# Optimization experiments

Hardware: AMD Instinct MI355X
Metric: run time of the kernel (lower is better)

## Reference

```python
import jax, jax.numpy as jnp
from jax import lax
import numpy as np

B = 8192   # samples
L = 32     # predicted chars per sample (num_chars[i])
M = 32     # target labels per sample (num_labels[i])
C = 96     # character classes


def _edit_trace(pred, tgt):
    """Levenshtein DP + backtrace for one sample.
    pred: [L] int, tgt: [M] int.
    Returns (ti, tj, valid) of length L+M: 1-based (i,j) positions of the
    diagonal (match/substitute) moves on the optimal edit path, as emitted by
    distance_and_trace; valid masks non-diagonal / out-of-path steps."""
    Ls, Ms = pred.shape[0], tgt.shape[0]
    cost = (pred[:, None] != tgt[None, :]).astype(jnp.int32)  # [L,M]
    row0 = jnp.arange(Ms + 1, dtype=jnp.int32)

    def row_step(prev, crow):
        first = prev[0] + 1
        def col_step(left, z):
            up, diag, c = z
            v = jnp.minimum(jnp.minimum(up + 1, left + 1), diag + c)
            return v, v
        _, rest = lax.scan(col_step, first, (prev[1:], prev[:-1], crow))
        new = jnp.concatenate([first[None], rest])
        return new, new

    _, rows = lax.scan(row_step, row0, cost)
    D = jnp.concatenate([row0[None, :], rows], axis=0)  # [L+1, M+1]

    def bt_step(carry, _):
        i, j = carry
        c = cost[jnp.maximum(i - 1, 0), jnp.maximum(j - 1, 0)]
        dij = D[i, j]
        diag = (i > 0) & (j > 0) & (D[i - 1, j - 1] + c == dij)
        up = (~diag) & (i > 0) & (D[i - 1, j] + 1 == dij)
        left = (~diag) & (~up) & (j > 0)
        ni = i - (diag | up).astype(jnp.int32)
        nj = j - (diag | left).astype(jnp.int32)
        return (ni, nj), (i, j, diag)

    (_, _), (ti, tj, valid) = lax.scan(
        bt_step, (jnp.int32(Ls), jnp.int32(Ms)), None, length=Ls + Ms)
    return ti, tj, valid


def _forward(x, y, num_chars, num_labels):
    b = num_chars.shape[0]
    c = x.shape[1]
    l = x.shape[0] // b
    m = y.shape[0] // b
    logits = x.reshape(b, l, c)          # [B,L,C]
    labels = y.reshape(b, m)             # [B,M]
    pred = jnp.argmax(logits, axis=-1)   # torch.max(x,1) indices
    ti, tj, valid = jax.vmap(_edit_trace)(pred, labels)  # [B, L+M] each
    logp = jax.nn.log_softmax(logits, axis=-1)
    xi = jnp.where(valid, ti - 1, 0)     # trace[:,0]-1 (+ per-sample offset via reshape)
    yi = jnp.where(valid, tj - 1, 0)     # trace[:,1]-1
    lab = jnp.take_along_axis(labels, yi, axis=1)                 # [B,L+M]
    lp = jnp.take_along_axis(logp, xi[..., None], axis=1)         # [B,L+M,C]
    ce = -jnp.take_along_axis(lp, lab[..., None], axis=2)[..., 0]  # [B,L+M]
    cnt = valid.sum(axis=1)
    per_sample = jnp.where(valid, ce, 0.0).sum(axis=1) / jnp.maximum(cnt, 1)
    nonempty = cnt > 0                   # attenuation: skip empty traces
    total = jnp.where(nonempty, per_sample, 0.0).sum()
    return total / nonempty.sum()


def setup_inputs() -> dict:
    key = jax.random.key(0)
    k1, k2 = jax.random.split(key)
    x = jax.random.normal(k1, (B * L, C), dtype=jnp.float32)
    y = jax.random.randint(k2, (B * M,), 0, C, dtype=jnp.int32)
    num_chars = jnp.full((B,), L, dtype=jnp.int32)
    num_labels = jnp.full((B,), M, dtype=jnp.int32)
    return {"x": x, "y": y, "num_chars": num_chars, "num_labels": num_labels}


def reference(x, y, num_chars, num_labels):
    return _forward(x, y, num_chars, num_labels)
```

## Files before the change

kernel.cpp:

```cpp
#include <hip/hip_runtime.h>
#include <stdint.h>

#define BNUM  8192
#define LROWS 32
#define MLAB  32
#define CCLS  96
#define WPB   4
#define SPW   2
#define SPB   (WPB*SPW)
#define NBLK  (BNUM/SPB)

__global__ __launch_bounds__(256, 4) void editloss_main(
    const float* __restrict__ x, const int* __restrict__ y,
    float* __restrict__ partial_sum, float* __restrict__ partial_cnt)
{
    __shared__ float  ceTab[SPB][LROWS * MLAB];
    __shared__ float2 lpS[SPB][LROWS];
    __shared__ float  psum[SPB];
    __shared__ float  pcnt[SPB];

    const int w    = threadIdx.x >> 6;
    const int lane = threadIdx.x & 63;
    const int g    = lane >> 5;
    const int u    = lane & 31;
    const int s    = w * SPW + g;
    const int sb   = blockIdx.x * SPB + s;

    const float* xs    = x + (size_t)sb * (LROWS * CCLS);
    const int    lab_u = y[sb * MLAB + u];

    float gbuf[LROWS];
    {
        const float* gcol = xs + lab_u;
#pragma unroll
        for (int r = 0; r < LROWS; ++r) gbuf[r] = gcol[r * CCLS];
    }

    {
        const float4* rowv = (const float4*)(xs + (size_t)u * CCLS);
        float mA = -1e30f, mB = -1e30f;
        int   iA = 0,      iB = 0;
        float sA = 0.f,    sB = 0.f;
#pragma unroll
        for (int k = 0; k < 12; ++k) {
            const float4 v = rowv[k];
            const int base = k * 4;
            if (v.x > mA) { mA = v.x; iA = base + 0; }
            if (v.y > mA) { mA = v.y; iA = base + 1; }
            if (v.z > mA) { mA = v.z; iA = base + 2; }
            if (v.w > mA) { mA = v.w; iA = base + 3; }
            sA += __expf(v.x) + __expf(v.y) + __expf(v.z) + __expf(v.w);
        }
#pragma unroll
        for (int k = 0; k < 12; ++k) {
            const float4 v = rowv[12 + k];
            const int base = 48 + k * 4;
            if (v.x > mB) { mB = v.x; iB = base + 0; }
            if (v.y > mB) { mB = v.y; iB = base + 1; }
            if (v.z > mB) { mB = v.z; iB = base + 2; }
            if (v.w > mB) { mB = v.w; iB = base + 3; }
            sB += __expf(v.x) + __expf(v.y) + __expf(v.z) + __expf(v.w);
        }
        const int   idx = (mB > mA) ? iB : iA;
        const float lse = __logf(sA + sB);
        lpS[s][u] = make_float2(lse, (float)idx);
    }
    asm volatile("s_waitcnt lgkmcnt(0)" ::: "memory");

#pragma unroll
    for (int r = 0; r < LROWS; ++r) {
        const float2 lp = lpS[s][r];
        const float  ce = lp.x - gbuf[r];
        ceTab[s][r * MLAB + u] = ((int)lp.y == lab_u) ? ce : -ce;
    }
    asm volatile("s_waitcnt lgkmcnt(0)" ::: "memory");

    const int j = u + 1;
    int   prevW = 0;   float prevCE = 0.f;
    int   diagW = 0;   float diagCE = 0.f;
#pragma unroll 4
    for (int d = 1; d <= LROWS + MLAB; ++d) {
        const int   lWs  = __shfl_up(prevW, 1);
        const float lCEs = __shfl_up(prevCE, 1);
        const int i = d - j;
        const int   lW  = (u == 0) ? max(i, 0)     : lWs;
        const float lCE = (u == 0) ? 0.f           : lCEs;
        const int   dW  = (u == 0) ? max(i - 1, 0) : diagW;
        const float dCE = (u == 0) ? 0.f           : diagCE;
        int curW; float curCE;
        if (i <= 0) {
            curW = j; curCE = 0.f;
        } else if (i > LROWS) {
            curW = prevW; curCE = prevCE;
        } else {
            const int uD = prevW & 255, uC = prevW >> 8;
            const int lD = lW & 255,    lC = lW >> 8;
            const int dD = dW & 255,    dC = dW >> 8;
            const float ct  = ceTab[s][(i - 1) * MLAB + u];
            const int   c   = (ct < 0.f) ? 1 : 0;
            const int nD = min(min(uD, lD) + 1, dD + c);
            const bool dg = (dD + c == nD);
            const bool up = !dg && (uD + 1 == nD);
            int nC; float nCE;
            if (dg)      { nC = dC + 1; nCE = dCE + fabsf(ct); }
            else if (up) { nC = uC;     nCE = prevCE;          }
            else         { nC = lC;     nCE = lCE;             }
            curW = nD | (nC << 8);
            curCE = nCE;
        }
        diagW = lWs; diagCE = lCEs;
        prevW = curW; prevCE = curCE;
    }

    if (u == 31) {
        const int cnt = prevW >> 8;
        psum[s] = (cnt > 0) ? prevCE / (float)cnt : 0.f;
        pcnt[s] = (cnt > 0) ? 1.f : 0.f;
    }
    __syncthreads();
    if (threadIdx.x == 0) {
        float ss = 0.f, cc = 0.f;
#pragma unroll
        for (int k = 0; k < SPB; ++k) { ss += psum[k]; cc += pcnt[k]; }
        partial_sum[blockIdx.x] = ss;
        partial_cnt[blockIdx.x] = cc;
    }
}

__global__ __launch_bounds__(256) void editloss_finalize(
    const float* __restrict__ partial_sum, const float* __restrict__ partial_cnt,
    float* __restrict__ out, int nblocks)
{
    float s = 0.f, c = 0.f;
    for (int k = threadIdx.x; k < nblocks; k += 256) {
        s += partial_sum[k];
        c += partial_cnt[k];
    }
#pragma unroll
    for (int d = 32; d >= 1; d >>= 1) {
        s += __shfl_xor(s, d);
        c += __shfl_xor(c, d);
    }
    __shared__ float ss[4], cc[4];
    const int w = threadIdx.x >> 6, lane = threadIdx.x & 63;
    if (lane == 0) { ss[w] = s; cc[w] = c; }
    __syncthreads();
    if (threadIdx.x == 0) {
        const float S  = ss[0] + ss[1] + ss[2] + ss[3];
        const float C2 = cc[0] + cc[1] + cc[2] + cc[3];
        out[0] = (C2 > 0.f) ? (S / C2) : 0.f;
    }
}

extern "C" void kernel_launch(void* const* d_in, const int* in_sizes, int n_in,
                              void* d_out, int out_size, void* d_ws, size_t ws_size,
                              hipStream_t stream) {
    const float* x = (const float*)d_in[0];
    const int*   y = (const int*)d_in[1];
    float* out = (float*)d_out;

    float* partial_sum = (float*)d_ws;
    float* partial_cnt = partial_sum + NBLK;

    editloss_main<<<NBLK, 256, 0, stream>>>(x, y, partial_sum, partial_cnt);
    editloss_finalize<<<1, 256, 0, stream>>>(partial_sum, partial_cnt, out, NBLK);
}
```

Before: 170.2 us.

## Prefetch row into registers, shrink blocks, write per-sample results without block sync

Loads each thread's full 96-float logit row into registers up front, together with the label-column gathers, so all global loads are issued before any compute. Blocks shrink from 4 to 2 wavefronts (128 threads), which halves shared memory per block and doubles the block count. The end-of-block __syncthreads reduction is dropped: each sample writes its own float2 to the workspace, and the finalize kernel reduces all 8192 entries. The register buffers raise VGPR pressure, which may lower occupancy, and finalize now reads more data.

Result: no change. 171.9 us (+1.0%).

```diff
diff --git a/kernel.cpp b/kernel.cpp
--- a/kernel.cpp
+++ b/kernel.cpp
@@ -5,19 +5,17 @@
 #define LROWS 32
 #define MLAB  32
 #define CCLS  96
-#define WPB   4
+#define WPB   2
 #define SPW   2
 #define SPB   (WPB*SPW)
 #define NBLK  (BNUM/SPB)
 
-__global__ __launch_bounds__(256, 4) void editloss_main(
+__global__ __launch_bounds__(128, 4) void editloss_main(
     const float* __restrict__ x, const int* __restrict__ y,
-    float* __restrict__ partial_sum, float* __restrict__ partial_cnt)
+    float2* __restrict__ out_ws)
 {
     __shared__ float  ceTab[SPB][LROWS * MLAB];
     __shared__ float2 lpS[SPB][LROWS];
-    __shared__ float  psum[SPB];
-    __shared__ float  pcnt[SPB];
 
     const int w    = threadIdx.x >> 6;
     const int lane = threadIdx.x & 63;
@@ -29,6 +27,11 @@
     const float* xs    = x + (size_t)sb * (LROWS * CCLS);
     const int    lab_u = y[sb * MLAB + u];
 
+    const float4* rowv = (const float4*)(xs + (size_t)u * CCLS);
+    float4 buf[24];
+#pragma unroll
+    for (int k = 0; k < 24; ++k) buf[k] = rowv[k];
+
     float gbuf[LROWS];
     {
         const float* gcol = xs + lab_u;
@@ -36,35 +39,38 @@
         for (int r = 0; r < LROWS; ++r) gbuf[r] = gcol[r * CCLS];
     }
 
-    {
-        const float4* rowv = (const float4*)(xs + (size_t)u * CCLS);
-        float mA = -1e30f, mB = -1e30f;
-        int   iA = 0,      iB = 0;
-        float sA = 0.f,    sB = 0.f;
+    float mA = -1e30f, mB = -1e30f;
+    int   iA = 0,      iB = 0;
+    float sA = 0.f,    sB = 0.f;
 #pragma unroll
-        for (int k = 0; k < 12; ++k) {
-            const float4 v = rowv[k];
-            const int base = k * 4;
-            if (v.x > mA) { mA = v.x; iA = base + 0; }
-            if (v.y > mA) { mA = v.y; iA = base + 1; }
-            if (v.z > mA) { mA = v.z; iA = base + 2; }
-            if (v.w > mA) { mA = v.w; iA = base + 3; }
-            sA += __expf(v.x) + __expf(v.y) + __expf(v.z) + __expf(v.w);
-        }
+    for (int k = 0; k < 12; ++k) {
+        const float4 v = buf[k];
+        const int base = k * 4;
+        if (v.x > mA) { mA = v.x; iA = base + 0; }
+        if (v.y > mA) { mA = v.y; iA = base + 1; }
+        if (v.z > mA) { mA = v.z; iA = base + 2; }
+        if (v.w > mA) { mA = v.w; iA = base + 3; }
+        sA += __expf(v.x) + __expf(v.y) + __expf(v.z) + __expf(v.w);
+    }
 #pragma unroll
-        for (int k = 0; k < 12; ++k) {
-            const float4 v = rowv[12 + k];
-            const int base = 48 + k * 4;
-            if (v.x > mB) { mB = v.x; iB = base + 0; }
-            if (v.y > mB) { mB = v.y; iB = base + 1; }
-            if (v.z > mB) { mB = v.z; iB = base + 2; }
-            if (v.w > mB) { mB = v.w; iB = base + 3; }
-            sB += __expf(v.x) + __expf(v.y) + __expf(v.z) + __expf(v.w);
-        }
-        const int   idx = (mB > mA) ? iB : iA;
-        const float lse = __logf(sA + sB);
-        lpS[s][u] = make_float2(lse, (float)idx);
+    for (int k = 0; k < 12; ++k) {
+        const float4 v = buf[12 + k];
+        const int base = 48 + k * 4;
+        if (v.x > mB) { mB = v.x; iB = base + 0; }
+        if (v.y > mB) { mB = v.y; iB = base + 1; }
+        if (v.z > mB) { mB = v.z; iB = base + 2; }
+        if (v.w > mB) { mB = v.w; iB = base + 3; }
+        sB += __expf(v.x) + __expf(v.y) + __expf(v.z) + __expf(v.w);
     }
+    const int   idx = (mB > mA) ? iB : iA;
+    const float lse = __logf(sA + sB);
+    lpS[s][u] = make_float2(lse, (float)idx);
+
+#pragma unroll
+    for (int r = 0; r < LROWS; r += 4)
+        asm volatile("" : "+v"(gbuf[r]), "+v"(gbuf[r+1]),
+                          "+v"(gbuf[r+2]), "+v"(gbuf[r+3]));
+
     asm volatile("s_waitcnt lgkmcnt(0)" ::: "memory");
 
 #pragma unroll
@@ -114,27 +120,18 @@
 
     if (u == 31) {
         const int cnt = prevW >> 8;
-        psum[s] = (cnt > 0) ? prevCE / (float)cnt : 0.f;
-        pcnt[s] = (cnt > 0) ? 1.f : 0.f;
-    }
-    __syncthreads();
-    if (threadIdx.x == 0) {
-        float ss = 0.f, cc = 0.f;
-#pragma unroll
-        for (int k = 0; k < SPB; ++k) { ss += psum[k]; cc += pcnt[k]; }
-        partial_sum[blockIdx.x] = ss;
-        partial_cnt[blockIdx.x] = cc;
+        out_ws[sb] = make_float2((cnt > 0) ? prevCE / (float)cnt : 0.f,
+                                 (cnt > 0) ? 1.f : 0.f);
     }
 }
 
 __global__ __launch_bounds__(256) void editloss_finalize(
-    const float* __restrict__ partial_sum, const float* __restrict__ partial_cnt,
-    float* __restrict__ out, int nblocks)
+    const float2* __restrict__ ws, float* __restrict__ out)
 {
     float s = 0.f, c = 0.f;
-    for (int k = threadIdx.x; k < nblocks; k += 256) {
-        s += partial_sum[k];
-        c += partial_cnt[k];
+    for (int k = threadIdx.x; k < BNUM; k += 256) {
+        const float2 v = ws[k];
+        s += v.x; c += v.y;
     }
 #pragma unroll
     for (int d = 32; d >= 1; d >>= 1) {
@@ -159,9 +156,8 @@
     const int*   y = (const int*)d_in[1];
     float* out = (float*)d_out;
 
-    float* partial_sum = (float*)d_ws;
-    float* partial_cnt = partial_sum + NBLK;
+    float2* per_sample = (float2*)d_ws;
 
-    editloss_main<<<NBLK, 256, 0, stream>>>(x, y, partial_sum, partial_cnt);
-    editloss_finalize<<<1, 256, 0, stream>>>(partial_sum, partial_cnt, out, NBLK);
+    editloss_main<<<NBLK, 128, 0, stream>>>(x, y, per_sample);
+    editloss_finalize<<<1, 256, 0, stream>>>(per_sample, out);
 }
```
